# Kernel optimization log

Measured on AMD Instinct MI355X. Metric: run time of the kernel, lower is better.

Reference implementation:

```python
import jax, jax.numpy as jnp
import numpy as np

NUM_HEADS = 16
HEAD_DIM = 128  # 2048 / 16


def setup_inputs() -> dict:
    key = jax.random.key(0)
    ks = jax.random.split(key, 5)
    B, S, D = 2, 2048, 2048
    scale = 1.0 / np.sqrt(D)
    return {
        "x": jax.random.normal(ks[0], (B, S, D), dtype=jnp.float32),
        "Wq": jax.random.normal(ks[1], (D, D), dtype=jnp.float32) * scale,
        "Wk": jax.random.normal(ks[2], (D, D), dtype=jnp.float32) * scale,
        "Wv": jax.random.normal(ks[3], (D, D), dtype=jnp.float32) * scale,
        "Wo": jax.random.normal(ks[4], (D, D), dtype=jnp.float32) * scale,
    }


def reference(x, Wq, Wk, Wv, Wo):
    B, S, D = x.shape
    H, Hd = NUM_HEADS, HEAD_DIM
    # nn.Linear(bias=False): y = x @ W.T
    q = (x @ Wq.T).reshape(B, S, H, Hd).transpose(0, 2, 1, 3)  # [B,H,S,Hd]
    k = (x @ Wk.T).reshape(B, S, H, Hd).transpose(0, 2, 1, 3)
    v = (x @ Wv.T).reshape(B, S, H, Hd).transpose(0, 2, 1, 3)
    scores = jnp.einsum("bhqd,bhkd->bhqk", q, k) / jnp.sqrt(jnp.float32(Hd))
    attn = jax.nn.softmax(scores, axis=-1)  # dropout p=0 (eval) -> identity
    out = jnp.einsum("bhqk,bhkd->bhqd", attn, v)  # [B,H,S,Hd]
    out = out.transpose(0, 2, 1, 3).reshape(B, S, D)
    out = out @ Wo.T
    return out
```

## Files before the change

### kernel.cpp

```cpp
#include <hip/hip_runtime.h>
#include <math.h>
#include <stdint.h>


#define DDIM 2048
#define SEQ  2048
#define NH   16
#define HD   128

typedef __attribute__((ext_vector_type(4))) float f32x4;
typedef __attribute__((ext_vector_type(16))) float f32x16;
typedef __attribute__((ext_vector_type(8))) __bf16 bf16x8;
typedef __attribute__((ext_vector_type(4))) unsigned int u32x4;
typedef __attribute__((ext_vector_type(2))) unsigned int u32x2;

#define MFMA_B16(a, b, c) __builtin_amdgcn_mfma_f32_16x16x32_bf16((a), (b), (c), 0, 0, 0)
#define MFMA32(a, b, c) __builtin_amdgcn_mfma_f32_32x32x16_bf16((a), (b), (c), 0, 0, 0)

__device__ __forceinline__ void async16(const void* g, void* l) {
  __builtin_amdgcn_global_load_lds(
      (const __attribute__((address_space(1))) unsigned int*)g,
      (__attribute__((address_space(3))) unsigned int*)l, 16, 0, 0);
}

__device__ __forceinline__ unsigned short f2bf(float f) {
  unsigned u = __builtin_bit_cast(unsigned, f);
  u += 0x7fffu + ((u >> 16) & 1u);
  return (unsigned short)(u >> 16);
}

__device__ __forceinline__ bf16x8 ldfrag(const unsigned short* p) {
  return __builtin_bit_cast(bf16x8, *(const u32x4*)p);
}

__device__ __forceinline__ void cvt_body(const float* __restrict__ s,
                                         unsigned short* __restrict__ d, int i) {
  const f32x4* sp = (const f32x4*)s;
  f32x4 a = sp[2 * i], b = sp[2 * i + 1];
  u32x4 o;
  o.x = ((unsigned)f2bf(a.y) << 16) | f2bf(a.x);
  o.y = ((unsigned)f2bf(a.w) << 16) | f2bf(a.z);
  o.z = ((unsigned)f2bf(b.y) << 16) | f2bf(b.x);
  o.w = ((unsigned)f2bf(b.w) << 16) | f2bf(b.z);
  ((u32x4*)d)[i] = o;
}

__global__ __launch_bounds__(256) void cvt_bf16_kernel(const float* __restrict__ s,
                                                       unsigned short* __restrict__ d) {
  cvt_body(s, d, blockIdx.x * 256 + threadIdx.x);
}

__global__ __launch_bounds__(256) void cvt_all_kernel(const float* __restrict__ x,
                                                      const float* __restrict__ wq,
                                                      const float* __restrict__ wk,
                                                      const float* __restrict__ wv,
                                                      const float* __restrict__ wo,
                                                      unsigned short* __restrict__ xb,
                                                      unsigned short* __restrict__ wqkv,
                                                      unsigned short* __restrict__ wob) {
  const int b = blockIdx.x;
  if (b < 4096) {
    cvt_body(x, xb, b * 256 + threadIdx.x);
  } else if (b < 10240) {
    const int wi = (b - 4096) >> 11, lb = (b - 4096) & 2047;
    const float* s = (wi == 0) ? wq : (wi == 1) ? wk : wv;
    cvt_body(s, wqkv + (size_t)wi * 4194304u, lb * 256 + threadIdx.x);
  } else {
    cvt_body(wo, wob, (b - 10240) * 256 + threadIdx.x);
  }
}

__global__ __launch_bounds__(256) void gemm_qkv(const unsigned short* __restrict__ A,
                                                const unsigned short* __restrict__ B,
                                                unsigned short* __restrict__ Oqk,
                                                unsigned short* __restrict__ Ovt,
                                                float alpha_q) {
  __shared__ unsigned short As[128 * 64];
  __shared__ unsigned short Bs[128 * 64];
  const int tid = threadIdx.x;
  const int lane = tid & 63, w = tid >> 6;
  const int l32 = lane & 31, half = lane >> 5;
  const int wm = (w >> 1) * 64, wn = (w & 1) * 64;
  const int bm = blockIdx.y * 128, bn = blockIdx.x * 128;

  f32x16 acc[2][2];
#pragma unroll
  for (int i = 0; i < 2; ++i)
#pragma unroll
    for (int j = 0; j < 2; ++j)
#pragma unroll
      for (int e = 0; e < 16; ++e) acc[i][j][e] = 0.f;

  const unsigned short* pa[4];
  const unsigned short* pbb[4];
  {
#pragma unroll
    for (int j = 0; j < 4; ++j) {
      const int row = j * 32 + (tid >> 3);
      const int cg = (tid & 7) ^ (row & 7) ^ ((row >> 3) & 7);
      pa[j] = A + (size_t)(bm + row) * DDIM + cg * 8;
      pbb[j] = B + (size_t)(bn + row) * DDIM + cg * 8;
    }
  }

  const int fr = (l32 & 7) ^ (l32 >> 3);

  for (int kt = 0; kt < 32; ++kt) {
    __syncthreads();
#pragma unroll
    for (int j = 0; j < 4; ++j) {
      async16(pa[j], &As[(j * 256 + tid) * 8]);
      pa[j] += 64;
      async16(pbb[j], &Bs[(j * 256 + tid) * 8]);
      pbb[j] += 64;
    }
    __syncthreads();
#pragma unroll
    for (int ks = 0; ks < 4; ++ks) {
      const int ph = ks * 2 + half;
      const int sl0 = (ph ^ fr) * 8;
      const int sl1 = (ph ^ fr ^ 4) * 8;
      bf16x8 af0 = ldfrag(&As[(wm + l32) * 64 + sl0]);
      bf16x8 af1 = ldfrag(&As[(wm + 32 + l32) * 64 + sl1]);
      bf16x8 bf0 = ldfrag(&Bs[(wn + l32) * 64 + sl0]);
      bf16x8 bf1 = ldfrag(&Bs[(wn + 32 + l32) * 64 + sl1]);
      acc[0][0] = MFMA32(af0, bf0, acc[0][0]);
      acc[0][1] = MFMA32(af0, bf1, acc[0][1]);
      acc[1][0] = MFMA32(af1, bf0, acc[1][0]);
      acc[1][1] = MFMA32(af1, bf1, acc[1][1]);
    }
  }

  const int seg = bn >> 11;
  const int bnl = bn & 2047;
  const float alpha = (seg == 0) ? alpha_q : 1.0f;
#pragma unroll
  for (int i = 0; i < 2; ++i) {
#pragma unroll
    for (int j = 0; j < 2; ++j) {
#pragma unroll
      for (int rg = 0; rg < 4; ++rg) {
        const int m0 = bm + wm + i * 32 + rg * 8 + half * 4;
        const float v0 = acc[i][j][rg * 4 + 0] * alpha;
        const float v1 = acc[i][j][rg * 4 + 1] * alpha;
        const float v2 = acc[i][j][rg * 4 + 2] * alpha;
        const float v3 = acc[i][j][rg * 4 + 3] * alpha;
        const int n = bnl + wn + j * 32 + l32;
        if (seg < 2) {
          unsigned short* O = Oqk + (size_t)seg * (4096u * 2048u);
          O[(size_t)(m0 + 0) * DDIM + n] = f2bf(v0);
          O[(size_t)(m0 + 1) * DDIM + n] = f2bf(v1);
          O[(size_t)(m0 + 2) * DDIM + n] = f2bf(v2);
          O[(size_t)(m0 + 3) * DDIM + n] = f2bf(v3);
        } else {
          const int bb = m0 >> 11, s0 = m0 & 2047;
          const int hh = n >> 7, dd = n & 127;
          u32x2 st;
          st.x = ((unsigned)f2bf(v1) << 16) | f2bf(v0);
          st.y = ((unsigned)f2bf(v3) << 16) | f2bf(v2);
          *(u32x2*)&Ovt[((size_t)((bb * NH + hh) * HD + dd)) * SEQ + s0] = st;
        }
      }
    }
  }
}

__global__ __launch_bounds__(256) void gemm_o64(const unsigned short* __restrict__ A,
                                                const unsigned short* __restrict__ B,
                                                float* __restrict__ Cf) {
  __shared__ unsigned short As[128 * 64];
  __shared__ unsigned short Bs[64 * 64];
  const int tid = threadIdx.x;
  const int lane = tid & 63, w = tid >> 6;
  const int l32 = lane & 31, half = lane >> 5;
  const int wm = (w >> 1) * 64, wn = (w & 1) * 32;
  const int bm = blockIdx.y * 128, bn = blockIdx.x * 64;

  f32x16 acc[2];
#pragma unroll
  for (int i = 0; i < 2; ++i)
#pragma unroll
    for (int e = 0; e < 16; ++e) acc[i][e] = 0.f;

  const unsigned short* pa[4];
  const unsigned short* pbb[2];
  {
#pragma unroll
    for (int j = 0; j < 4; ++j) {
      const int row = j * 32 + (tid >> 3);
      const int cg = (tid & 7) ^ (row & 7) ^ ((row >> 3) & 7);
      pa[j] = A + (size_t)(bm + row) * DDIM + cg * 8;
      if (j < 2) pbb[j] = B + (size_t)(bn + row) * DDIM + cg * 8;
    }
  }

  const int fr = (l32 & 7) ^ (l32 >> 3);
  const int fb = fr ^ ((wn >> 3) & 4);

  for (int kt = 0; kt < 32; ++kt) {
    __syncthreads();
#pragma unroll
    for (int j = 0; j < 4; ++j) {
      async16(pa[j], &As[(j * 256 + tid) * 8]);
      pa[j] += 64;
      if (j < 2) {
        async16(pbb[j], &Bs[(j * 256 + tid) * 8]);
        pbb[j] += 64;
      }
    }
    __syncthreads();
#pragma unroll
    for (int ks = 0; ks < 4; ++ks) {
      const int ph = ks * 2 + half;
      bf16x8 af0 = ldfrag(&As[(wm + l32) * 64 + (ph ^ fr) * 8]);
      bf16x8 af1 = ldfrag(&As[(wm + 32 + l32) * 64 + (ph ^ fr ^ 4) * 8]);
      bf16x8 bf0 = ldfrag(&Bs[(wn + l32) * 64 + (ph ^ fb) * 8]);
      acc[0] = MFMA32(af0, bf0, acc[0]);
      acc[1] = MFMA32(af1, bf0, acc[1]);
    }
  }

#pragma unroll
  for (int i = 0; i < 2; ++i) {
#pragma unroll
    for (int rg = 0; rg < 4; ++rg) {
      const int m0 = bm + wm + i * 32 + rg * 8 + half * 4;
      const int n = bn + wn + l32;
      Cf[(size_t)(m0 + 0) * DDIM + n] = acc[i][rg * 4 + 0];
      Cf[(size_t)(m0 + 1) * DDIM + n] = acc[i][rg * 4 + 1];
      Cf[(size_t)(m0 + 2) * DDIM + n] = acc[i][rg * 4 + 2];
      Cf[(size_t)(m0 + 3) * DDIM + n] = acc[i][rg * 4 + 3];
    }
  }
}

__global__ __launch_bounds__(512) void attn_kernel(const unsigned short* __restrict__ qb,
                                                   const unsigned short* __restrict__ kb,
                                                   const unsigned short* __restrict__ vtb,
                                                   unsigned short* __restrict__ ab) {
  __shared__ unsigned short Ks[64 * 128];
  __shared__ unsigned short Vts[128 * 64];
  __shared__ unsigned short Pw[2][8 * 16 * 40];
  const int tid = threadIdx.x;
  const int w = tid >> 6, lane = tid & 63;
  const int quad = lane >> 4, l16 = lane & 15;
  const int qt = blockIdx.x, bh = blockIdx.y;
  const int b = bh >> 4, h = bh & 15;
  const int qrow = qt * 128 + w * 16 + l16;

  const unsigned short* qp = qb + ((size_t)(b * SEQ + qrow)) * DDIM + h * HD;
  bf16x8 qf[4];
#pragma unroll
  for (int ks = 0; ks < 4; ++ks) qf[ks] = ldfrag(qp + ks * 32 + quad * 8);

  f32x4 ot[8];
#pragma unroll
  for (int i = 0; i < 8; i++) ot[i] = f32x4{0.f, 0.f, 0.f, 0.f};
  float sumacc = 0.f;

  const unsigned short* kp[2];
  const unsigned short* vp[2];
  {
    const size_t kbase = ((size_t)(b * SEQ)) * DDIM + h * HD;
    const size_t vbase = ((size_t)((b * NH + h) * HD)) * SEQ;
#pragma unroll
    for (int j = 0; j < 2; ++j) {
      const int key = j * 32 + (tid >> 4), cgk = (tid & 15) ^ (key & 15);
      kp[j] = kb + kbase + (size_t)key * DDIM + cgk * 8;
      const int dd = j * 64 + (tid >> 3), cgv = (tid & 7) ^ (dd & 7);
      vp[j] = vtb + vbase + (size_t)dd * SEQ + cgv * 8;
    }
  }
  unsigned short* pw0 = &Pw[0][w * 640];
  unsigned short* pw1 = &Pw[1][w * 640];

  for (int kt = 0; kt < SEQ / 64; ++kt) {
    __syncthreads();
#pragma unroll
    for (int j = 0; j < 2; ++j) {
      async16(kp[j], &Ks[(j * 512 + tid) * 8]);
      kp[j] += (size_t)64 * DDIM;
      async16(vp[j], &Vts[(j * 512 + tid) * 8]);
      vp[j] += 64;
    }
    __syncthreads();
    f32x4 s[4];
#pragma unroll
    for (int t = 0; t < 4; ++t) s[t] = f32x4{0.f, 0.f, 0.f, 0.f};
#pragma unroll
    for (int ks = 0; ks < 4; ++ks) {
      const int sl = ((ks * 4 + quad) ^ l16) * 8;
#pragma unroll
      for (int t = 0; t < 4; ++t) {
        bf16x8 a = ldfrag(&Ks[(t * 16 + l16) * 128 + sl]);
        s[t] = MFMA_B16(a, qf[ks], s[t]);
      }
    }
    f32x4 p[4];
#pragma unroll
    for (int t = 0; t < 4; ++t) {
      p[t].x = __builtin_amdgcn_exp2f(s[t].x);
      p[t].y = __builtin_amdgcn_exp2f(s[t].y);
      p[t].z = __builtin_amdgcn_exp2f(s[t].z);
      p[t].w = __builtin_amdgcn_exp2f(s[t].w);
      sumacc += (p[t].x + p[t].y) + (p[t].z + p[t].w);
    }
    bf16x8 pb0, pb1;
    {
      u32x2 w0, w1, w2, w3;
      w0.x = ((unsigned)f2bf(p[0].y) << 16) | f2bf(p[0].x);
      w0.y = ((unsigned)f2bf(p[0].w) << 16) | f2bf(p[0].z);
      w1.x = ((unsigned)f2bf(p[1].y) << 16) | f2bf(p[1].x);
      w1.y = ((unsigned)f2bf(p[1].w) << 16) | f2bf(p[1].z);
      w2.x = ((unsigned)f2bf(p[2].y) << 16) | f2bf(p[2].x);
      w2.y = ((unsigned)f2bf(p[2].w) << 16) | f2bf(p[2].z);
      w3.x = ((unsigned)f2bf(p[3].y) << 16) | f2bf(p[3].x);
      w3.y = ((unsigned)f2bf(p[3].w) << 16) | f2bf(p[3].z);
      *(u32x2*)&pw0[l16 * 40 + quad * 4] = w0;
      *(u32x2*)&pw0[l16 * 40 + 16 + quad * 4] = w1;
      *(u32x2*)&pw1[l16 * 40 + quad * 4] = w2;
      *(u32x2*)&pw1[l16 * 40 + 16 + quad * 4] = w3;
      asm volatile("s_waitcnt lgkmcnt(0)" ::: "memory");
      __builtin_amdgcn_sched_barrier(0);
      pb0 = ldfrag(&pw0[l16 * 40 + quad * 8]);
      pb1 = ldfrag(&pw1[l16 * 40 + quad * 8]);
    }
#pragma unroll
    for (int mt = 0; mt < 8; ++mt) {
      bf16x8 vf0 = ldfrag(&Vts[(mt * 16 + l16) * 64 + (quad ^ (l16 & 7)) * 8]);
      ot[mt] = MFMA_B16(vf0, pb0, ot[mt]);
      bf16x8 vf1 = ldfrag(&Vts[(mt * 16 + l16) * 64 + ((4 + quad) ^ (l16 & 7)) * 8]);
      ot[mt] = MFMA_B16(vf1, pb1, ot[mt]);
    }
  }
  float total = sumacc;
  total += __shfl_xor(total, 16);
  total += __shfl_xor(total, 32);
  const float inv = 1.0f / total;
  unsigned short* op = ab + ((size_t)(b * SEQ + qrow)) * DDIM + h * HD;
#pragma unroll
  for (int mt = 0; mt < 8; ++mt) {
    f32x4 v = ot[mt] * inv;
    u32x2 st;
    st.x = ((unsigned)f2bf(v.y) << 16) | f2bf(v.x);
    st.y = ((unsigned)f2bf(v.w) << 16) | f2bf(v.z);
    *(u32x2*)&op[mt * 16 + quad * 4] = st;
  }
}

extern "C" void kernel_launch(void* const* d_in, const int* in_sizes, int n_in,
                              void* d_out, int out_size, void* d_ws, size_t ws_size,
                              hipStream_t stream) {
  (void)in_sizes; (void)n_in; (void)out_size;
  const float* x = (const float*)d_in[0];
  const float* Wq = (const float*)d_in[1];
  const float* Wk = (const float*)d_in[2];
  const float* Wv = (const float*)d_in[3];
  const float* Wo = (const float*)d_in[4];

  char* ws = (char*)d_ws;
  unsigned short* xb = (unsigned short*)(ws);
  unsigned short* wqkv = (unsigned short*)(ws + 16777216);
  unsigned short* qb = (unsigned short*)(ws + 41943040);
  unsigned short* kb = (unsigned short*)(ws + 58720256);
  unsigned short* vtb = (unsigned short*)(ws + 75497472);
  const bool big = ws_size >= 100663296ull;
  unsigned short* wob = big ? (unsigned short*)(ws + 92274688) : wqkv;

  const float alpha_q = 1.44269504088896341f / sqrtf(128.0f);

  if (big) {
    cvt_all_kernel<<<dim3(12288), 256, 0, stream>>>(x, Wq, Wk, Wv, Wo, xb, wqkv, wob);
    gemm_qkv<<<dim3(48, 32), 256, 0, stream>>>(xb, wqkv, qb, vtb, alpha_q);
  } else {
    cvt_all_kernel<<<dim3(10240), 256, 0, stream>>>(x, Wq, Wk, Wv, Wo, xb, wqkv, wob);
    gemm_qkv<<<dim3(48, 32), 256, 0, stream>>>(xb, wqkv, qb, vtb, alpha_q);
    cvt_bf16_kernel<<<dim3(2048), 256, 0, stream>>>(Wo, wob);
  }

  attn_kernel<<<dim3(16, 32), 512, 0, stream>>>(qb, kb, vtb, xb);

  gemm_o64<<<dim3(32, 32), 256, 0, stream>>>(xb, wob, (float*)d_out);
}
```

Baseline: 373.9 us.

## Give each attention wave two query row tiles to reuse K/V fragments

The attention block drops from 8 waves to 4, and each wave now handles 32 query rows as two 16-row halves. Every K fragment and V fragment read from LDS feeds two MFMAs instead of one, which halves LDS reads per unit of work and also halves the per-thread share of the cooperative tile loads. The cost is roughly double the accumulator and score registers per thread, with launch bounds (256,2) set to hold occupancy. Fewer waves per block may also hide less latency around the barriers.

```diff
diff --git a/kernel.cpp b/kernel.cpp
--- a/kernel.cpp
+++ b/kernel.cpp
@@ -234,117 +234,154 @@
   }
 }
 
-__global__ __launch_bounds__(512) void attn_kernel(const unsigned short* __restrict__ qb,
-                                                   const unsigned short* __restrict__ kb,
-                                                   const unsigned short* __restrict__ vtb,
-                                                   unsigned short* __restrict__ ab) {
+__global__ __launch_bounds__(256, 2) void attn_kernel(
+    const unsigned short* __restrict__ qb, const unsigned short* __restrict__ kb,
+    const unsigned short* __restrict__ vtb, unsigned short* __restrict__ ab) {
   __shared__ unsigned short Ks[64 * 128];
   __shared__ unsigned short Vts[128 * 64];
-  __shared__ unsigned short Pw[2][8 * 16 * 40];
+  __shared__ unsigned short Pw[4][4 * 16 * 40];
   const int tid = threadIdx.x;
   const int w = tid >> 6, lane = tid & 63;
   const int quad = lane >> 4, l16 = lane & 15;
   const int qt = blockIdx.x, bh = blockIdx.y;
   const int b = bh >> 4, h = bh & 15;
-  const int qrow = qt * 128 + w * 16 + l16;
-
-  const unsigned short* qp = qb + ((size_t)(b * SEQ + qrow)) * DDIM + h * HD;
-  bf16x8 qf[4];
-#pragma unroll
-  for (int ks = 0; ks < 4; ++ks) qf[ks] = ldfrag(qp + ks * 32 + quad * 8);
-
-  f32x4 ot[8];
-#pragma unroll
-  for (int i = 0; i < 8; i++) ot[i] = f32x4{0.f, 0.f, 0.f, 0.f};
-  float sumacc = 0.f;
-
-  const unsigned short* kp[2];
-  const unsigned short* vp[2];
+  const int qrow0 = qt * 128 + w * 32 + l16;
+
+  bf16x8 qf[2][4];
+#pragma unroll
+  for (int qh = 0; qh < 2; ++qh) {
+    const unsigned short* qp =
+        qb + ((size_t)(b * SEQ + qrow0 + qh * 16)) * DDIM + h * HD;
+#pragma unroll
+    for (int ks = 0; ks < 4; ++ks) qf[qh][ks] = ldfrag(qp + ks * 32 + quad * 8);
+  }
+
+  f32x4 ot[2][8];
+#pragma unroll
+  for (int qh = 0; qh < 2; ++qh)
+#pragma unroll
+    for (int i = 0; i < 8; i++) ot[qh][i] = f32x4{0.f, 0.f, 0.f, 0.f};
+  float sum0 = 0.f, sum1 = 0.f;
+
+  const unsigned short* kp[4];
+  const unsigned short* vp[4];
   {
     const size_t kbase = ((size_t)(b * SEQ)) * DDIM + h * HD;
     const size_t vbase = ((size_t)((b * NH + h) * HD)) * SEQ;
 #pragma unroll
-    for (int j = 0; j < 2; ++j) {
-      const int key = j * 32 + (tid >> 4), cgk = (tid & 15) ^ (key & 15);
+    for (int j = 0; j < 4; ++j) {
+      const int slot = j * 256 + tid;
+      const int key = slot >> 4, cgk = (slot & 15) ^ (key & 15);
       kp[j] = kb + kbase + (size_t)key * DDIM + cgk * 8;
-      const int dd = j * 64 + (tid >> 3), cgv = (tid & 7) ^ (dd & 7);
+      const int dd = slot >> 3, cgv = (slot & 7) ^ (dd & 7);
       vp[j] = vtb + vbase + (size_t)dd * SEQ + cgv * 8;
     }
   }
-  unsigned short* pw0 = &Pw[0][w * 640];
-  unsigned short* pw1 = &Pw[1][w * 640];
+  unsigned short* pw00 = &Pw[0][w * 640];
+  unsigned short* pw01 = &Pw[1][w * 640];
+  unsigned short* pw10 = &Pw[2][w * 640];
+  unsigned short* pw11 = &Pw[3][w * 640];
 
   for (int kt = 0; kt < SEQ / 64; ++kt) {
     __syncthreads();
 #pragma unroll
-    for (int j = 0; j < 2; ++j) {
-      async16(kp[j], &Ks[(j * 512 + tid) * 8]);
+    for (int j = 0; j < 4; ++j) {
+      async16(kp[j], &Ks[(j * 256 + tid) * 8]);
       kp[j] += (size_t)64 * DDIM;
-      async16(vp[j], &Vts[(j * 512 + tid) * 8]);
+      async16(vp[j], &Vts[(j * 256 + tid) * 8]);
       vp[j] += 64;
     }
     __syncthreads();
-    f32x4 s[4];
-#pragma unroll
-    for (int t = 0; t < 4; ++t) s[t] = f32x4{0.f, 0.f, 0.f, 0.f};
+    f32x4 s0[4], s1[4];
+#pragma unroll
+    for (int t = 0; t < 4; ++t) {
+      s0[t] = f32x4{0.f, 0.f, 0.f, 0.f};
+      s1[t] = f32x4{0.f, 0.f, 0.f, 0.f};
+    }
 #pragma unroll
     for (int ks = 0; ks < 4; ++ks) {
       const int sl = ((ks * 4 + quad) ^ l16) * 8;
 #pragma unroll
       for (int t = 0; t < 4; ++t) {
         bf16x8 a = ldfrag(&Ks[(t * 16 + l16) * 128 + sl]);
-        s[t] = MFMA_B16(a, qf[ks], s[t]);
+        s0[t] = MFMA_B16(a, qf[0][ks], s0[t]);
+        s1[t] = MFMA_B16(a, qf[1][ks], s1[t]);
       }
     }
-    f32x4 p[4];
+    f32x4 p0[4], p1[4];
 #pragma unroll
     for (int t = 0; t < 4; ++t) {
-      p[t].x = __builtin_amdgcn_exp2f(s[t].x);
-      p[t].y = __builtin_amdgcn_exp2f(s[t].y);
-      p[t].z = __builtin_amdgcn_exp2f(s[t].z);
-      p[t].w = __builtin_amdgcn_exp2f(s[t].w);
-      sumacc += (p[t].x + p[t].y) + (p[t].z + p[t].w);
-    }
-    bf16x8 pb0, pb1;
+      p0[t].x = __builtin_amdgcn_exp2f(s0[t].x);
+      p0[t].y = __builtin_amdgcn_exp2f(s0[t].y);
+      p0[t].z = __builtin_amdgcn_exp2f(s0[t].z);
+      p0[t].w = __builtin_amdgcn_exp2f(s0[t].w);
+      sum0 += (p0[t].x + p0[t].y) + (p0[t].z + p0[t].w);
+      p1[t].x = __builtin_amdgcn_exp2f(s1[t].x);
+      p1[t].y = __builtin_amdgcn_exp2f(s1[t].y);
+      p1[t].z = __builtin_amdgcn_exp2f(s1[t].z);
+      p1[t].w = __builtin_amdgcn_exp2f(s1[t].w);
+      sum1 += (p1[t].x + p1[t].y) + (p1[t].z + p1[t].w);
+    }
+    bf16x8 pb00, pb01, pb10, pb11;
     {
-      u32x2 w0, w1, w2, w3;
-      w0.x = ((unsigned)f2bf(p[0].y) << 16) | f2bf(p[0].x);
-      w0.y = ((unsigned)f2bf(p[0].w) << 16) | f2bf(p[0].z);
-      w1.x = ((unsigned)f2bf(p[1].y) << 16) | f2bf(p[1].x);
-      w1.y = ((unsigned)f2bf(p[1].w) << 16) | f2bf(p[1].z);
-      w2.x = ((unsigned)f2bf(p[2].y) << 16) | f2bf(p[2].x);
-      w2.y = ((unsigned)f2bf(p[2].w) << 16) | f2bf(p[2].z);
-      w3.x = ((unsigned)f2bf(p[3].y) << 16) | f2bf(p[3].x);
-      w3.y = ((unsigned)f2bf(p[3].w) << 16) | f2bf(p[3].z);
-      *(u32x2*)&pw0[l16 * 40 + quad * 4] = w0;
-      *(u32x2*)&pw0[l16 * 40 + 16 + quad * 4] = w1;
-      *(u32x2*)&pw1[l16 * 40 + quad * 4] = w2;
-      *(u32x2*)&pw1[l16 * 40 + 16 + quad * 4] = w3;
+      u32x2 a0, a1, a2, a3, b0, b1, b2, b3;
+      a0.x = ((unsigned)f2bf(p0[0].y) << 16) | f2bf(p0[0].x);
+      a0.y = ((unsigned)f2bf(p0[0].w) << 16) | f2bf(p0[0].z);
+      a1.x = ((unsigned)f2bf(p0[1].y) << 16) | f2bf(p0[1].x);
+      a1.y = ((unsigned)f2bf(p0[1].w) << 16) | f2bf(p0[1].z);
+      a2.x = ((unsigned)f2bf(p0[2].y) << 16) | f2bf(p0[2].x);
+      a2.y = ((unsigned)f2bf(p0[2].w) << 16) | f2bf(p0[2].z);
+      a3.x = ((unsigned)f2bf(p0[3].y) << 16) | f2bf(p0[3].x);
+      a3.y = ((unsigned)f2bf(p0[3].w) << 16) | f2bf(p0[3].z);
+      b0.x = ((unsigned)f2bf(p1[0].y) << 16) | f2bf(p1[0].x);
+      b0.y = ((unsigned)f2bf(p1[0].w) << 16) | f2bf(p1[0].z);
+      b1.x = ((unsigned)f2bf(p1[1].y) << 16) | f2bf(p1[1].x);
+      b1.y = ((unsigned)f2bf(p1[1].w) << 16) | f2bf(p1[1].z);
+      b2.x = ((unsigned)f2bf(p1[2].y) << 16) | f2bf(p1[2].x);
+      b2.y = ((unsigned)f2bf(p1[2].w) << 16) | f2bf(p1[2].z);
+      b3.x = ((unsigned)f2bf(p1[3].y) << 16) | f2bf(p1[3].x);
+      b3.y = ((unsigned)f2bf(p1[3].w) << 16) | f2bf(p1[3].z);
+      *(u32x2*)&pw00[l16 * 40 + quad * 4] = a0;
+      *(u32x2*)&pw00[l16 * 40 + 16 + quad * 4] = a1;
+      *(u32x2*)&pw01[l16 * 40 + quad * 4] = a2;
+      *(u32x2*)&pw01[l16 * 40 + 16 + quad * 4] = a3;
+      *(u32x2*)&pw10[l16 * 40 + quad * 4] = b0;
+      *(u32x2*)&pw10[l16 * 40 + 16 + quad * 4] = b1;
+      *(u32x2*)&pw11[l16 * 40 + quad * 4] = b2;
+      *(u32x2*)&pw11[l16 * 40 + 16 + quad * 4] = b3;
       asm volatile("s_waitcnt lgkmcnt(0)" ::: "memory");
       __builtin_amdgcn_sched_barrier(0);
-      pb0 = ldfrag(&pw0[l16 * 40 + quad * 8]);
-      pb1 = ldfrag(&pw1[l16 * 40 + quad * 8]);
+      pb00 = ldfrag(&pw00[l16 * 40 + quad * 8]);
+      pb01 = ldfrag(&pw01[l16 * 40 + quad * 8]);
+      pb10 = ldfrag(&pw10[l16 * 40 + quad * 8]);
+      pb11 = ldfrag(&pw11[l16 * 40 + quad * 8]);
     }
 #pragma unroll
     for (int mt = 0; mt < 8; ++mt) {
       bf16x8 vf0 = ldfrag(&Vts[(mt * 16 + l16) * 64 + (quad ^ (l16 & 7)) * 8]);
-      ot[mt] = MFMA_B16(vf0, pb0, ot[mt]);
       bf16x8 vf1 = ldfrag(&Vts[(mt * 16 + l16) * 64 + ((4 + quad) ^ (l16 & 7)) * 8]);
-      ot[mt] = MFMA_B16(vf1, pb1, ot[mt]);
-    }
-  }
-  float total = sumacc;
-  total += __shfl_xor(total, 16);
-  total += __shfl_xor(total, 32);
-  const float inv = 1.0f / total;
-  unsigned short* op = ab + ((size_t)(b * SEQ + qrow)) * DDIM + h * HD;
-#pragma unroll
-  for (int mt = 0; mt < 8; ++mt) {
-    f32x4 v = ot[mt] * inv;
-    u32x2 st;
-    st.x = ((unsigned)f2bf(v.y) << 16) | f2bf(v.x);
-    st.y = ((unsigned)f2bf(v.w) << 16) | f2bf(v.z);
-    *(u32x2*)&op[mt * 16 + quad * 4] = st;
+      ot[0][mt] = MFMA_B16(vf0, pb00, ot[0][mt]);
+      ot[0][mt] = MFMA_B16(vf1, pb01, ot[0][mt]);
+      ot[1][mt] = MFMA_B16(vf0, pb10, ot[1][mt]);
+      ot[1][mt] = MFMA_B16(vf1, pb11, ot[1][mt]);
+    }
+  }
+#pragma unroll
+  for (int qh = 0; qh < 2; ++qh) {
+    float total = (qh == 0) ? sum0 : sum1;
+    total += __shfl_xor(total, 16);
+    total += __shfl_xor(total, 32);
+    const float inv = 1.0f / total;
+    unsigned short* op =
+        ab + ((size_t)(b * SEQ + qrow0 + qh * 16)) * DDIM + h * HD;
+#pragma unroll
+    for (int mt = 0; mt < 8; ++mt) {
+      f32x4 v = ot[qh][mt] * inv;
+      u32x2 st;
+      st.x = ((unsigned)f2bf(v.y) << 16) | f2bf(v.x);
+      st.y = ((unsigned)f2bf(v.w) << 16) | f2bf(v.z);
+      *(u32x2*)&op[mt * 16 + quad * 4] = st;
+    }
   }
 }
 
@@ -378,7 +415,7 @@
     cvt_bf16_kernel<<<dim3(2048), 256, 0, stream>>>(Wo, wob);
   }
 
-  attn_kernel<<<dim3(16, 32), 512, 0, stream>>>(qb, kb, vtb, xb);
+  attn_kernel<<<dim3(16, 32), 256, 0, stream>>>(qb, kb, vtb, xb);
 
   gemm_o64<<<dim3(32, 32), 256, 0, stream>>>(xb, wob, (float*)d_out);
 }
```

New measurement: 381.9 us. 1.02x slower.
